# Performance work log

Hardware: AMD Instinct MI355X
Metric: run time of the kernel (lower is better)

The kernel has to match this reference:

```python
import jax, jax.numpy as jnp
import numpy as np

BETA = 1.0  # write blending coefficient (beta in original module)


def ste(x):
    # Binarize with straight-through estimator: forward (x>0.5), backward identity.
    b = (x > 0.5).astype(x.dtype)
    return x + jax.lax.stop_gradient(b - x)


def setup_inputs() -> dict:
    key = jax.random.key(0)
    k0, k1, k2 = jax.random.split(key, 3)
    B, H, W, HID = 8, 512, 512, 64
    f0 = jax.random.uniform(k0, (B, 1, H, W), dtype=jnp.float32)
    W1 = jax.random.normal(k1, (9, HID), dtype=jnp.float32) * (1.0 / np.sqrt(9.0))
    b1 = jnp.zeros((HID,), dtype=jnp.float32)
    W2 = jax.random.normal(k2, (HID, 1), dtype=jnp.float32) * (1.0 / np.sqrt(HID))
    b2 = jnp.zeros((1,), dtype=jnp.float32)
    return {"f0": f0, "W1": W1, "b1": b1, "W2": W2, "b2": b2, "T": 16}


def reference(f0, W1, b1, W2, b2, T):
    B, _, H, Wd = f0.shape

    def step(f, _):
        f_read = ste(f)                                            # (B,1,H,W) binarized read
        pad = jnp.pad(f_read, ((0, 0), (0, 0), (1, 1), (1, 1)), mode="wrap")
        # 3x3 neighborhoods, row-major top-left -> bottom-right: (B,H,W,9)
        neigh = jnp.stack(
            [pad[:, 0, i:i + H, j:j + Wd] for i in range(3) for j in range(3)],
            axis=-1,
        )
        h = jax.nn.relu(jnp.einsum("bhwn,nk->bhwk", neigh, W1) + b1)
        logits = (jnp.einsum("bhwk,ko->bhwo", h, W2) + b2)[..., 0]  # (B,H,W)
        w_bits = ste(jax.nn.sigmoid(logits))[:, None]               # (B,1,H,W)
        f_new = (1.0 - BETA) * f + BETA * w_bits
        return f_new, f_new

    _, rest = jax.lax.scan(step, f0, None, length=T - 1)
    fields = jnp.concatenate([f0[None], rest], axis=0)  # (T,B,1,H,W)
    return fields
```

## Files before the change

kernel.cpp:

```cpp
#include <hip/hip_runtime.h>

#define HH 512
#define WW 512
#define WPR 16
#define RO 8
#define HALO 15
#define ROWS (RO + 2 * HALO)
#define OW 8
#define TW 10

#define STEP_BARRIER() do {                                   \
    asm volatile("s_waitcnt lgkmcnt(0)" ::: "memory");        \
    __builtin_amdgcn_s_barrier();                             \
    __builtin_amdgcn_sched_barrier(0);                        \
} while (0)

__global__ __launch_bounds__(512) void init_pack(const float* __restrict__ f0,
                                                 const float* __restrict__ W1,
                                                 const float* __restrict__ b1,
                                                 const float* __restrict__ W2,
                                                 const float* __restrict__ b2,
                                                 int hid,
                                                 float* __restrict__ out,
                                                 unsigned long long* __restrict__ field,
                                                 unsigned int* __restrict__ lutg) {
    __shared__ unsigned int rule[512];
    const int tid = threadIdx.x;
    int c = blockIdx.x * 512 + tid;
    float v = f0[c];
    out[c] = v;
    unsigned long long m = __ballot(v > 0.5f);
    if ((tid & 63) == 0) field[c >> 6] = m;

    if (blockIdx.x == 0) {
        {
            int p = tid;
            float logit = b2[0];
            for (int k = 0; k < hid; ++k) {
                float a = b1[k];
#pragma unroll
                for (int nn = 0; nn < 9; ++nn)
                    if (p & (1 << nn)) a += W1[nn * hid + k];
                logit += fmaxf(a, 0.0f) * W2[k];
            }
            rule[p] = (logit > 0.0f) ? 1u : 0u;
        }
        __syncthreads();
        if (tid < 256) {
            unsigned int wv = 0;
#pragma unroll
            for (int k = 0; k < 16; ++k) {
                unsigned int e = (unsigned int)tid * 16u + k;
                unsigned int u = e & 15u, mm = (e >> 4) & 15u, d = (e >> 8) & 15u;
                unsigned int i0 = (u & 7u) | ((mm & 7u) << 3) | ((d & 7u) << 6);
                unsigned int i1 = (u >> 1) | ((mm >> 1) << 3) | ((d >> 1) << 6);
                wv |= (rule[i0] | (rule[i1] << 1)) << (2 * k);
            }
            lutg[tid] = wv;
        }
    }
}

__global__ __launch_bounds__(512) void mega(const unsigned int* __restrict__ field,
                                            const unsigned int* __restrict__ lutg,
                                            float* __restrict__ out,
                                            int n, int T) {
    __shared__ unsigned int lutp[256];
    __shared__ unsigned int bufA[ROWS * TW];
    __shared__ unsigned int bufB[ROWS * TW];

    const int tid = threadIdx.x;
    const int cg = blockIdx.x & 1;
    const int rg = (blockIdx.x >> 1) & 63;
    const int b  = blockIdx.x >> 7;
    const int r0 = rg * RO;
    const int q0 = cg * OW;
    const int c0 = cg * (OW * 32);

    if (tid < 256) lutp[tid] = lutg[tid];
    {
        const unsigned int* F = field + b * (HH * WPR);
        for (int i = tid; i < ROWS * TW; i += 512) {
            int l = i / TW, tw = i - l * TW;
            int g  = (r0 - HALO + l) & (HH - 1);
            int gw = (q0 - 1 + tw) & (WPR - 1);
            bufA[i] = F[g * WPR + gw];
        }
    }
    __syncthreads();

    unsigned int* oldb = bufA;
    unsigned int* newb = bufB;
    float* outb = out + (size_t)b * (HH * WW);

    for (int t = 1; t < T; ++t) {
        const int hi = ROWS - t;
        const int lq = tid / TW;
        const int w  = tid - lq * TW;
        const int l  = t + lq;
        if (l < hi) {
            const unsigned int* Ru = oldb + (l - 1) * TW;
            const unsigned int* Rm = oldb + l * TW;
            const unsigned int* Rd = oldb + (l + 1) * TW;
            const int wl = (w == 0) ? 0 : w - 1;
            const int wn = (w == TW - 1) ? TW - 1 : w + 1;
            unsigned long long eu = ((((unsigned long long)Ru[wn] << 32) | Ru[w]) << 1) | (Ru[wl] >> 31);
            unsigned long long em = ((((unsigned long long)Rm[wn] << 32) | Rm[w]) << 1) | (Rm[wl] >> 31);
            unsigned long long ed = ((((unsigned long long)Rd[wn] << 32) | Rd[w]) << 1) | (Rd[wl] >> 31);
            unsigned int ow = 0;
#pragma unroll
            for (int j = 0; j < 16; ++j) {
                unsigned int idx = (unsigned int)((eu >> (2 * j)) & 15ull)
                                 | ((unsigned int)((em >> (2 * j)) & 15ull) << 4)
                                 | ((unsigned int)((ed >> (2 * j)) & 15ull) << 8);
                ow |= ((lutp[idx >> 4] >> ((idx & 15u) * 2)) & 3u) << (2 * j);
            }
            newb[l * TW + w] = ow;
        }
        STEP_BARRIER();

        float* outt = outb + (size_t)t * n;
        {
            int cell = tid * 4;
            int lr  = cell >> 8;
            int col = cell & 255;
            unsigned int wv = newb[(HALO + lr) * TW + 1 + (col >> 5)];
            unsigned int nib = (wv >> (col & 31)) & 15u;
            float4 v;
            v.x = (float)(nib & 1u);
            v.y = (float)((nib >> 1) & 1u);
            v.z = (float)((nib >> 2) & 1u);
            v.w = (float)(nib >> 3);
            *(float4*)(outt + (size_t)(r0 + lr) * WW + c0 + col) = v;
        }
        unsigned int* tmp = oldb; oldb = newb; newb = tmp;
    }
}

extern "C" void kernel_launch(void* const* d_in, const int* in_sizes, int n_in,
                              void* d_out, int out_size, void* d_ws, size_t ws_size,
                              hipStream_t stream) {
    const float* f0 = (const float*)d_in[0];
    const float* W1 = (const float*)d_in[1];
    const float* b1 = (const float*)d_in[2];
    const float* W2 = (const float*)d_in[3];
    const float* b2 = (const float*)d_in[4];
    float* out = (float*)d_out;

    const int n = in_sizes[0];
    const int hid = in_sizes[2];
    const int T = out_size / n;
    const int B = n / (HH * WW);

    char* ws = (char*)d_ws;
    unsigned int* lutg = (unsigned int*)ws;
    unsigned long long* fld = (unsigned long long*)(ws + 1024);

    init_pack<<<n / 512, 512, 0, stream>>>(f0, W1, b1, W2, b2, hid, out, fld, lutg);
    mega<<<B * (HH / RO) * 2, 512, 0, stream>>>((const unsigned int*)fld, lutg,
                                                out, n, T);
}
```

Before: 63.36 us.

## Compute two output rows per thread with 16-bit LUT and taller tiles

Replaces the 12-bit-input lookup table that yields 2 cells with a 16-bit-input table (4 rows × 4 columns of bits) that yields a 2×2 block, so each thread produces two rows per step from four loaded rows. The row tile grows from 8 to 16 so the fixed 15-row halo is a smaller share of the work, halving the number of blocks. The table grows to 32 KB of shared memory per block, built by 64 init blocks and copied in by every block, which raises LDS pressure and may lower occupancy and add random LDS bank conflicts.

New measurement: 62.88 us. Within noise of the previous version (-0.8%).

```diff
diff --git a/kernel.cpp b/kernel.cpp
--- a/kernel.cpp
+++ b/kernel.cpp
@@ -3,7 +3,7 @@
 #define HH 512
 #define WW 512
 #define WPR 16
-#define RO 8
+#define RO 16
 #define HALO 15
 #define ROWS (RO + 2 * HALO)
 #define OW 8
@@ -23,7 +23,7 @@
                                                  int hid,
                                                  float* __restrict__ out,
                                                  unsigned long long* __restrict__ field,
-                                                 unsigned int* __restrict__ lutg) {
+                                                 unsigned int* __restrict__ lut16g) {
     __shared__ unsigned int rule[512];
     const int tid = threadIdx.x;
     int c = blockIdx.x * 512 + tid;
@@ -32,7 +32,7 @@
     unsigned long long m = __ballot(v > 0.5f);
     if ((tid & 63) == 0) field[c >> 6] = m;
 
-    if (blockIdx.x == 0) {
+    if (blockIdx.x < 64) {
         {
             int p = tid;
             float logit = b2[0];
@@ -46,38 +46,43 @@
             rule[p] = (logit > 0.0f) ? 1u : 0u;
         }
         __syncthreads();
-        if (tid < 256) {
+        if (tid < 128) {
+            int word = blockIdx.x * 128 + tid;
             unsigned int wv = 0;
 #pragma unroll
-            for (int k = 0; k < 16; ++k) {
-                unsigned int e = (unsigned int)tid * 16u + k;
-                unsigned int u = e & 15u, mm = (e >> 4) & 15u, d = (e >> 8) & 15u;
-                unsigned int i0 = (u & 7u) | ((mm & 7u) << 3) | ((d & 7u) << 6);
-                unsigned int i1 = (u >> 1) | ((mm >> 1) << 3) | ((d >> 1) << 6);
-                wv |= (rule[i0] | (rule[i1] << 1)) << (2 * k);
+            for (int k = 0; k < 8; ++k) {
+                unsigned int e = (unsigned int)word * 8u + k;
+                unsigned int a = e & 15u, b = (e >> 4) & 15u;
+                unsigned int cc = (e >> 8) & 15u, d = (e >> 12) & 15u;
+                unsigned int bit0 = rule[(a & 7u) | ((b & 7u) << 3) | ((cc & 7u) << 6)];
+                unsigned int bit1 = rule[((a >> 1) & 7u) | (((b >> 1) & 7u) << 3) | (((cc >> 1) & 7u) << 6)];
+                unsigned int bit2 = rule[(b & 7u) | ((cc & 7u) << 3) | ((d & 7u) << 6)];
+                unsigned int bit3 = rule[((b >> 1) & 7u) | (((cc >> 1) & 7u) << 3) | (((d >> 1) & 7u) << 6)];
+                wv |= (bit0 | (bit1 << 1) | (bit2 << 2) | (bit3 << 3)) << (4 * k);
             }
-            lutg[tid] = wv;
+            lut16g[word] = wv;
         }
     }
 }
 
 __global__ __launch_bounds__(512) void mega(const unsigned int* __restrict__ field,
-                                            const unsigned int* __restrict__ lutg,
+                                            const unsigned int* __restrict__ lut16g,
                                             float* __restrict__ out,
                                             int n, int T) {
-    __shared__ unsigned int lutp[256];
+    __shared__ alignas(16) unsigned int lut16[8192];
     __shared__ unsigned int bufA[ROWS * TW];
     __shared__ unsigned int bufB[ROWS * TW];
 
     const int tid = threadIdx.x;
     const int cg = blockIdx.x & 1;
-    const int rg = (blockIdx.x >> 1) & 63;
-    const int b  = blockIdx.x >> 7;
+    const int rg = (blockIdx.x >> 1) & 31;
+    const int b  = blockIdx.x >> 6;
     const int r0 = rg * RO;
     const int q0 = cg * OW;
     const int c0 = cg * (OW * 32);
 
-    if (tid < 256) lutp[tid] = lutg[tid];
+    for (int i = tid; i < 2048; i += 512)
+        ((uint4*)lut16)[i] = ((const uint4*)lut16g)[i];
     {
         const unsigned int* F = field + b * (HH * WPR);
         for (int i = tid; i < ROWS * TW; i += 512) {
@@ -94,34 +99,41 @@
     float* outb = out + (size_t)b * (HH * WW);
 
     for (int t = 1; t < T; ++t) {
-        const int hi = ROWS - t;
-        const int lq = tid / TW;
-        const int w  = tid - lq * TW;
-        const int l  = t + lq;
-        if (l < hi) {
-            const unsigned int* Ru = oldb + (l - 1) * TW;
-            const unsigned int* Rm = oldb + l * TW;
-            const unsigned int* Rd = oldb + (l + 1) * TW;
+        const int npairs = 23 - t;
+        if (tid < npairs * TW) {
+            const int pr = tid / TW;
+            const int w  = tid - pr * TW;
+            const int l  = t + 2 * pr;
+            const unsigned int* Ra = oldb + (l - 1) * TW;
+            const unsigned int* Rb = oldb + l * TW;
+            const unsigned int* Rc = oldb + (l + 1) * TW;
+            const unsigned int* Rd = oldb + (l + 2) * TW;
             const int wl = (w == 0) ? 0 : w - 1;
             const int wn = (w == TW - 1) ? TW - 1 : w + 1;
-            unsigned long long eu = ((((unsigned long long)Ru[wn] << 32) | Ru[w]) << 1) | (Ru[wl] >> 31);
-            unsigned long long em = ((((unsigned long long)Rm[wn] << 32) | Rm[w]) << 1) | (Rm[wl] >> 31);
+            unsigned long long ea = ((((unsigned long long)Ra[wn] << 32) | Ra[w]) << 1) | (Ra[wl] >> 31);
+            unsigned long long eb = ((((unsigned long long)Rb[wn] << 32) | Rb[w]) << 1) | (Rb[wl] >> 31);
+            unsigned long long ec = ((((unsigned long long)Rc[wn] << 32) | Rc[w]) << 1) | (Rc[wl] >> 31);
             unsigned long long ed = ((((unsigned long long)Rd[wn] << 32) | Rd[w]) << 1) | (Rd[wl] >> 31);
-            unsigned int ow = 0;
+            unsigned int owb = 0, owc = 0;
 #pragma unroll
             for (int j = 0; j < 16; ++j) {
-                unsigned int idx = (unsigned int)((eu >> (2 * j)) & 15ull)
-                                 | ((unsigned int)((em >> (2 * j)) & 15ull) << 4)
-                                 | ((unsigned int)((ed >> (2 * j)) & 15ull) << 8);
-                ow |= ((lutp[idx >> 4] >> ((idx & 15u) * 2)) & 3u) << (2 * j);
+                unsigned int idx = (unsigned int)((ea >> (2 * j)) & 15ull)
+                                 | ((unsigned int)((eb >> (2 * j)) & 15ull) << 4)
+                                 | ((unsigned int)((ec >> (2 * j)) & 15ull) << 8)
+                                 | ((unsigned int)((ed >> (2 * j)) & 15ull) << 12);
+                unsigned int ent = (lut16[idx >> 3] >> ((idx & 7u) * 4)) & 15u;
+                owb |= (ent & 3u) << (2 * j);
+                owc |= ((ent >> 2) & 3u) << (2 * j);
             }
-            newb[l * TW + w] = ow;
+            newb[l * TW + w] = owb;
+            newb[(l + 1) * TW + w] = owc;
         }
         STEP_BARRIER();
 
         float* outt = outb + (size_t)t * n;
-        {
-            int cell = tid * 4;
+#pragma unroll
+        for (int rep = 0; rep < 2; ++rep) {
+            int cell = (rep * 512 + tid) * 4;
             int lr  = cell >> 8;
             int col = cell & 255;
             unsigned int wv = newb[(HALO + lr) * TW + 1 + (col >> 5)];
@@ -153,10 +165,10 @@
     const int B = n / (HH * WW);
 
     char* ws = (char*)d_ws;
-    unsigned int* lutg = (unsigned int*)ws;
-    unsigned long long* fld = (unsigned long long*)(ws + 1024);
+    unsigned int* lut16g = (unsigned int*)ws;
+    unsigned long long* fld = (unsigned long long*)(ws + 32768);
 
-    init_pack<<<n / 512, 512, 0, stream>>>(f0, W1, b1, W2, b2, hid, out, fld, lutg);
-    mega<<<B * (HH / RO) * 2, 512, 0, stream>>>((const unsigned int*)fld, lutg,
+    init_pack<<<n / 512, 512, 0, stream>>>(f0, W1, b1, W2, b2, hid, out, fld, lut16g);
+    mega<<<B * (HH / RO) * 2, 512, 0, stream>>>((const unsigned int*)fld, lut16g,
                                                 out, n, T);
 }
```

## Fuse field packing and rule LUT construction into the main stencil kernel

Applied to the files above, without the earlier changes.

Removes the separate init_pack kernel. Every block now evaluates the 512-entry MLP rule table and builds the packed LUT itself, then reads its haloed tile of f0 directly as floats, binarizes it with ballots into shared memory, and writes its own interior of timestep 0. This drops one kernel launch and the round trip of the packed field through global memory. In exchange, every block repeats the 64-hidden MLP evaluation, and the halo rows are read as 32-bit floats instead of packed bits, roughly 4.75x the tile area.

Result: slower. 102.2 us (+61.4%).

```diff
diff --git a/kernel.cpp b/kernel.cpp
--- a/kernel.cpp
+++ b/kernel.cpp
@@ -2,12 +2,12 @@
 
 #define HH 512
 #define WW 512
-#define WPR 16
 #define RO 8
 #define HALO 15
 #define ROWS (RO + 2 * HALO)
 #define OW 8
 #define TW 10
+#define TCOLS (TW * 32)
 
 #define STEP_BARRIER() do {                                   \
     asm volatile("s_waitcnt lgkmcnt(0)" ::: "memory");        \
@@ -15,56 +15,14 @@
     __builtin_amdgcn_sched_barrier(0);                        \
 } while (0)
 
-__global__ __launch_bounds__(512) void init_pack(const float* __restrict__ f0,
-                                                 const float* __restrict__ W1,
-                                                 const float* __restrict__ b1,
-                                                 const float* __restrict__ W2,
-                                                 const float* __restrict__ b2,
-                                                 int hid,
-                                                 float* __restrict__ out,
-                                                 unsigned long long* __restrict__ field,
-                                                 unsigned int* __restrict__ lutg) {
+__global__ __launch_bounds__(512) void mega(const float* __restrict__ f0,
+                                            const float* __restrict__ W1,
+                                            const float* __restrict__ b1,
+                                            const float* __restrict__ W2,
+                                            const float* __restrict__ b2,
+                                            int hid, float* __restrict__ out,
+                                            int n, int T) {
     __shared__ unsigned int rule[512];
-    const int tid = threadIdx.x;
-    int c = blockIdx.x * 512 + tid;
-    float v = f0[c];
-    out[c] = v;
-    unsigned long long m = __ballot(v > 0.5f);
-    if ((tid & 63) == 0) field[c >> 6] = m;
-
-    if (blockIdx.x == 0) {
-        {
-            int p = tid;
-            float logit = b2[0];
-            for (int k = 0; k < hid; ++k) {
-                float a = b1[k];
-#pragma unroll
-                for (int nn = 0; nn < 9; ++nn)
-                    if (p & (1 << nn)) a += W1[nn * hid + k];
-                logit += fmaxf(a, 0.0f) * W2[k];
-            }
-            rule[p] = (logit > 0.0f) ? 1u : 0u;
-        }
-        __syncthreads();
-        if (tid < 256) {
-            unsigned int wv = 0;
-#pragma unroll
-            for (int k = 0; k < 16; ++k) {
-                unsigned int e = (unsigned int)tid * 16u + k;
-                unsigned int u = e & 15u, mm = (e >> 4) & 15u, d = (e >> 8) & 15u;
-                unsigned int i0 = (u & 7u) | ((mm & 7u) << 3) | ((d & 7u) << 6);
-                unsigned int i1 = (u >> 1) | ((mm >> 1) << 3) | ((d >> 1) << 6);
-                wv |= (rule[i0] | (rule[i1] << 1)) << (2 * k);
-            }
-            lutg[tid] = wv;
-        }
-    }
-}
-
-__global__ __launch_bounds__(512) void mega(const unsigned int* __restrict__ field,
-                                            const unsigned int* __restrict__ lutg,
-                                            float* __restrict__ out,
-                                            int n, int T) {
     __shared__ unsigned int lutp[256];
     __shared__ unsigned int bufA[ROWS * TW];
     __shared__ unsigned int bufB[ROWS * TW];
@@ -74,17 +32,49 @@
     const int rg = (blockIdx.x >> 1) & 63;
     const int b  = blockIdx.x >> 7;
     const int r0 = rg * RO;
-    const int q0 = cg * OW;
     const int c0 = cg * (OW * 32);
 
-    if (tid < 256) lutp[tid] = lutg[tid];
     {
-        const unsigned int* F = field + b * (HH * WPR);
-        for (int i = tid; i < ROWS * TW; i += 512) {
-            int l = i / TW, tw = i - l * TW;
-            int g  = (r0 - HALO + l) & (HH - 1);
-            int gw = (q0 - 1 + tw) & (WPR - 1);
-            bufA[i] = F[g * WPR + gw];
+        int p = tid;
+        float logit = b2[0];
+        for (int k = 0; k < hid; ++k) {
+            float a = b1[k];
+#pragma unroll
+            for (int nn = 0; nn < 9; ++nn)
+                if (p & (1 << nn)) a += W1[nn * hid + k];
+            logit += fmaxf(a, 0.0f) * W2[k];
+        }
+        rule[p] = (logit > 0.0f) ? 1u : 0u;
+    }
+    __syncthreads();
+
+    if (tid < 256) {
+        unsigned int wv = 0;
+#pragma unroll
+        for (int k = 0; k < 16; ++k) {
+            unsigned int e = (unsigned int)tid * 16u + k;
+            unsigned int u = e & 15u, mm = (e >> 4) & 15u, d = (e >> 8) & 15u;
+            unsigned int i0 = (u & 7u) | ((mm & 7u) << 3) | ((d & 7u) << 6);
+            unsigned int i1 = (u >> 1) | ((mm >> 1) << 3) | ((d >> 1) << 6);
+            wv |= (rule[i0] | (rule[i1] << 1)) << (2 * k);
+        }
+        lutp[tid] = wv;
+    }
+
+    {
+        const float* f0b = f0 + (size_t)b * (HH * WW);
+        float* out0 = out + (size_t)b * (HH * WW);
+        const int lane = tid & 63;
+        for (int i = tid; i < ROWS * TCOLS; i += 512) {
+            int l = i / TCOLS, c = i - l * TCOLS;
+            int gr = (r0 - HALO + l) & (HH - 1);
+            int gc = (c0 - 32 + c) & (WW - 1);
+            float v = f0b[(size_t)gr * WW + gc];
+            unsigned long long m = __ballot(v > 0.5f);
+            if (lane == 0)  bufA[l * TW + (c >> 5)] = (unsigned int)m;
+            if (lane == 32) bufA[l * TW + (c >> 5)] = (unsigned int)(m >> 32);
+            if (l >= HALO && l < HALO + RO && c >= 32 && c < 32 + 256)
+                out0[(size_t)gr * WW + gc] = v;
         }
     }
     __syncthreads();
@@ -152,11 +142,5 @@
     const int T = out_size / n;
     const int B = n / (HH * WW);
 
-    char* ws = (char*)d_ws;
-    unsigned int* lutg = (unsigned int*)ws;
-    unsigned long long* fld = (unsigned long long*)(ws + 1024);
-
-    init_pack<<<n / 512, 512, 0, stream>>>(f0, W1, b1, W2, b2, hid, out, fld, lutg);
-    mega<<<B * (HH / RO) * 2, 512, 0, stream>>>((const unsigned int*)fld, lutg,
-                                                out, n, T);
+    mega<<<B * (HH / RO) * 2, 512, 0, stream>>>(f0, W1, b1, W2, b2, hid, out, n, T);
 }
```

## Split evolution and float expansion into separate kernels via packed bit frames

Applied to the files above, without the earlier changes.

The fused kernel used to write float4 output inside its time loop, with barriers between steps. Now the evolve kernel stores only packed bit words per frame to the workspace. A separate expand kernel then turns all frames into floats with a fully parallel grid. This takes the large global stores out of the barrier-bound stencil loop, at the cost of an extra launch and a round trip of the packed frames through workspace memory. It hardcodes 8 batches and 15 frames in FRAME_WORDS and the expand grid.

Measured after the change: 81.51 us. 28.7% more time.

```diff
diff --git a/kernel.cpp b/kernel.cpp
--- a/kernel.cpp
+++ b/kernel.cpp
@@ -8,6 +8,7 @@
 #define ROWS (RO + 2 * HALO)
 #define OW 8
 #define TW 10
+#define FRAME_WORDS (8 * HH * WPR)
 
 #define STEP_BARRIER() do {                                   \
     asm volatile("s_waitcnt lgkmcnt(0)" ::: "memory");        \
@@ -61,10 +62,10 @@
     }
 }
 
-__global__ __launch_bounds__(512) void mega(const unsigned int* __restrict__ field,
-                                            const unsigned int* __restrict__ lutg,
-                                            float* __restrict__ out,
-                                            int n, int T) {
+__global__ __launch_bounds__(512) void evolve(const unsigned int* __restrict__ field,
+                                              const unsigned int* __restrict__ lutg,
+                                              unsigned int* __restrict__ fields,
+                                              int T) {
     __shared__ unsigned int lutp[256];
     __shared__ unsigned int bufA[ROWS * TW];
     __shared__ unsigned int bufB[ROWS * TW];
@@ -75,7 +76,6 @@
     const int b  = blockIdx.x >> 7;
     const int r0 = rg * RO;
     const int q0 = cg * OW;
-    const int c0 = cg * (OW * 32);
 
     if (tid < 256) lutp[tid] = lutg[tid];
     {
@@ -91,7 +91,6 @@
 
     unsigned int* oldb = bufA;
     unsigned int* newb = bufB;
-    float* outb = out + (size_t)b * (HH * WW);
 
     for (int t = 1; t < T; ++t) {
         const int hi = ROWS - t;
@@ -116,25 +115,27 @@
                 ow |= ((lutp[idx >> 4] >> ((idx & 15u) * 2)) & 3u) << (2 * j);
             }
             newb[l * TW + w] = ow;
+            if (l >= HALO && l < HALO + RO && w >= 1 && w <= OW)
+                fields[(size_t)(t - 1) * FRAME_WORDS + b * (HH * WPR)
+                       + (size_t)(r0 + l - HALO) * WPR + (q0 + w - 1)] = ow;
         }
         STEP_BARRIER();
-
-        float* outt = outb + (size_t)t * n;
-        {
-            int cell = tid * 4;
-            int lr  = cell >> 8;
-            int col = cell & 255;
-            unsigned int wv = newb[(HALO + lr) * TW + 1 + (col >> 5)];
-            unsigned int nib = (wv >> (col & 31)) & 15u;
-            float4 v;
-            v.x = (float)(nib & 1u);
-            v.y = (float)((nib >> 1) & 1u);
-            v.z = (float)((nib >> 2) & 1u);
-            v.w = (float)(nib >> 3);
-            *(float4*)(outt + (size_t)(r0 + lr) * WW + c0 + col) = v;
-        }
         unsigned int* tmp = oldb; oldb = newb; newb = tmp;
     }
+}
+
+__global__ __launch_bounds__(512) void expand(const unsigned int* __restrict__ fields,
+                                              float* __restrict__ out, int n) {
+    const int f  = blockIdx.x >> 10;
+    const int g4 = ((blockIdx.x & 1023) << 9) + threadIdx.x;
+    unsigned int wv = fields[(size_t)f * FRAME_WORDS + (g4 >> 3)];
+    unsigned int nib = (wv >> ((g4 & 7) * 4)) & 15u;
+    float4 v;
+    v.x = (float)(nib & 1u);
+    v.y = (float)((nib >> 1) & 1u);
+    v.z = (float)((nib >> 2) & 1u);
+    v.w = (float)(nib >> 3);
+    ((float4*)out)[(size_t)(f + 1) * (n >> 2) + g4] = v;
 }
 
 extern "C" void kernel_launch(void* const* d_in, const int* in_sizes, int n_in,
@@ -155,8 +156,10 @@
     char* ws = (char*)d_ws;
     unsigned int* lutg = (unsigned int*)ws;
     unsigned long long* fld = (unsigned long long*)(ws + 1024);
+    unsigned int* frames = (unsigned int*)(ws + 1024 + (size_t)(n / 8));
 
     init_pack<<<n / 512, 512, 0, stream>>>(f0, W1, b1, W2, b2, hid, out, fld, lutg);
-    mega<<<B * (HH / RO) * 2, 512, 0, stream>>>((const unsigned int*)fld, lutg,
-                                                out, n, T);
+    evolve<<<B * (HH / RO) * 2, 512, 0, stream>>>((const unsigned int*)fld, lutg,
+                                                  frames, T);
+    expand<<<15 * 1024, 512, 0, stream>>>(frames, out, n);
 }
```
